# Optimization experiments

Measured on AMD Instinct MI355X. Metric: run time of the kernel, lower is better.

The kernel has to match this reference:

```python
import jax, jax.numpy as jnp
import numpy as np

EPS = 1e-5  # torch BatchNorm default

def _conv(x, w, pad):
    return jax.lax.conv_general_dilated(x, w, window_strides=(1, 1), padding=pad,
                                        dimension_numbers=('NCHW', 'OIHW', 'NCHW'))

def _bn(x, g, b, m, v):
    # eval-mode BatchNorm2d over channel axis 1 of NCHW
    scale = g / jnp.sqrt(v + EPS)
    return x * scale[None, :, None, None] + (b - m * scale)[None, :, None, None]

def _bn1d(x, g, b, m, v):
    scale = g / jnp.sqrt(v + EPS)
    return x * scale[None, :] + (b - m * scale)[None, :]

def _prelu(x, a):
    # torch PReLU with num_parameters=1 (scalar slope, init 0.25)
    return jnp.where(x >= 0, x, a * x)

def setup_inputs():
    key = jax.random.key(0)
    ks = jax.random.split(key, 10)
    B, H, W = 256, 600, 19
    C1, C2 = 40, 40
    x = jax.random.normal(ks[0], (B, H, W), jnp.float32)
    w1 = jax.random.normal(ks[1], (C1, 1, 29, 1), jnp.float32) * 0.1
    w2 = jax.random.normal(ks[2], (C2, C1, 1, 19), jnp.float32) * 0.1
    fc1_w = jax.random.uniform(ks[3], (80, 1560), jnp.float32, -0.005, 0.005)
    fc2_w = jax.random.uniform(ks[4], (2, 80), jnp.float32, -0.005, 0.005)
    def bn_params(k, n):
        k1, k2 = jax.random.split(k)
        return (jnp.ones((n,), jnp.float32), jnp.zeros((n,), jnp.float32),
                jax.random.normal(k1, (n,), jnp.float32) * 0.1,
                jax.random.uniform(k2, (n,), jnp.float32, 0.5, 1.5))
    bn1_g, bn1_b, bn1_m, bn1_v = bn_params(ks[5], C1)
    bn2_g, bn2_b, bn2_m, bn2_v = bn_params(ks[6], C2)
    bn3_g, bn3_b, bn3_m, bn3_v = bn_params(ks[7], 80)
    a1 = jnp.full((1,), 0.25, jnp.float32)
    a2 = jnp.full((1,), 0.25, jnp.float32)
    a3 = jnp.full((1,), 0.25, jnp.float32)
    return dict(x=x, w1=w1, bn1_g=bn1_g, bn1_b=bn1_b, bn1_m=bn1_m, bn1_v=bn1_v, a1=a1,
                w2=w2, bn2_g=bn2_g, bn2_b=bn2_b, bn2_m=bn2_m, bn2_v=bn2_v, a2=a2,
                fc1_w=fc1_w, bn3_g=bn3_g, bn3_b=bn3_b, bn3_m=bn3_m, bn3_v=bn3_v, a3=a3,
                fc2_w=fc2_w)

def reference(x, w1, bn1_g, bn1_b, bn1_m, bn1_v, a1,
              w2, bn2_g, bn2_b, bn2_m, bn2_v, a2,
              fc1_w, bn3_g, bn3_b, bn3_m, bn3_v, a3, fc2_w):
    h = x[:, None, :, :]                                  # [B,1,600,19]
    # conv1: inputs NOT binarized, weights sign-binarized
    h = _conv(h, jnp.sign(w1), [(14, 14), (0, 0)])         # [B,40,600,19]
    h = _prelu(_bn(h, bn1_g, bn1_b, bn1_m, bn1_v), a1)
    # conv2: inputs and weights binarized
    h = _conv(jnp.sign(h), jnp.sign(w2), [(0, 0), (0, 0)])  # [B,40,600,1]
    h = _prelu(_bn(h, bn2_g, bn2_b, bn2_m, bn2_v), a2)
    # AvgPool2d kernel (30,1) stride (15,1)
    h = jax.lax.reduce_window(h, 0.0, jax.lax.add, (1, 1, 30, 1), (1, 1, 15, 1), 'VALID') / 30.0  # [B,40,39,1]
    h = h.reshape(h.shape[0], -1)                          # [B,1560]
    # fc1: binarized input/weight; BatchNorm1d; PReLU; dropout is identity in eval
    h = jnp.sign(h) @ jnp.sign(fc1_w).T                    # [B,80]
    h = _prelu(_bn1d(h, bn3_g, bn3_b, bn3_m, bn3_v), a3)
    out = jnp.sign(h) @ jnp.sign(fc2_w).T                  # [B,2]
    return out
```

## Files before the change

kernel.cpp:

```cpp
#include <hip/hip_runtime.h>
#include <stdint.h>

#define B_ 256
#define H_ 600
#define W_ 19
#define C1_ 40
#define C2_ 40
#define KH_ 29
#define PAD_ 14
#define NW_ 760
#define NWORDS_ 12
#define NJ_ 39
#define FIN_ 1560
#define FOUT_ 80
#define FCW_ 25
#define XST2 328
#define HS_ 300

typedef float v2f __attribute__((ext_vector_type(2)));

__device__ __forceinline__ float fsgn(float x){ return (x > 0.f) ? 1.f : ((x < 0.f) ? -1.f : 0.f); }
__device__ __forceinline__ int8_t isgn(float x){ return (int8_t)((x > 0.f) - (x < 0.f)); }

__global__ void k0_setup(const float* __restrict__ w1, const float* __restrict__ w2,
                         const float* __restrict__ fc1w, const float* __restrict__ fc2w,
                         const float* __restrict__ g1, const float* __restrict__ b1,
                         const float* __restrict__ m1, const float* __restrict__ v1,
                         const float* __restrict__ g2, const float* __restrict__ b2,
                         const float* __restrict__ m2, const float* __restrict__ v2,
                         const float* __restrict__ g3, const float* __restrict__ b3,
                         const float* __restrict__ m3, const float* __restrict__ v3,
                         float* __restrict__ w1s, uint64_t* __restrict__ w2m,
                         uint64_t* __restrict__ fc1p, int8_t* __restrict__ fc2s,
                         float* __restrict__ bnp)
{
  int tid = blockIdx.x * blockDim.x + threadIdx.x;
  int np  = gridDim.x * blockDim.x;
  int lane = threadIdx.x & 63;
  int gw   = tid >> 6;
  int nw   = np >> 6;

  for (int i = tid; i < C1_*KH_; i += np) w1s[i] = fsgn(w1[i]);

  for (int v = gw; v < C2_*NWORDS_; v += nw){
    int c2 = v / NWORDS_, wd = v % NWORDS_;
    int idx = wd*64 + lane;
    float val = 0.f;
    if (idx < NW_){
      int c1 = idx % 40, w = idx / 40;
      val = w2[c2*NW_ + c1*W_ + w];
    }
    unsigned long long m = __ballot(val > 0.f);
    if (lane == 0) w2m[c2*NWORDS_ + wd] = m;
  }
  for (int v = gw; v < FOUT_*2*FCW_; v += nw){
    int o = v / (2*FCW_), r = v % (2*FCW_);
    int neg = r / FCW_, wd = r % FCW_;
    int e = wd*64 + lane;
    float val = (e < FIN_) ? fc1w[o*FIN_ + e] : 0.f;
    unsigned long long m = __ballot(neg ? (val < 0.f) : (val > 0.f));
    if (lane == 0) fc1p[o*(2*FCW_) + r] = m;
  }
  for (int i = tid; i < 2*FOUT_; i += np) fc2s[i] = isgn(fc2w[i]);
  for (int i = tid; i < C1_; i += np){
    float s = __fdiv_rn(g1[i], __fsqrt_rn(__fadd_rn(v1[i], 1e-5f)));
    bnp[i] = s; bnp[40+i] = __fsub_rn(b1[i], __fmul_rn(m1[i], s));
  }
  for (int i = tid; i < C2_; i += np){
    float s = __fdiv_rn(g2[i], __fsqrt_rn(__fadd_rn(v2[i], 1e-5f)));
    bnp[80+i] = s; bnp[120+i] = __fsub_rn(b2[i], __fmul_rn(m2[i], s));
  }
  for (int i = tid; i < FOUT_; i += np){
    float s = __fdiv_rn(g3[i], __fsqrt_rn(__fadd_rn(v3[i], 1e-5f)));
    bnp[160+i] = s; bnp[240+i] = __fsub_rn(b3[i], __fmul_rn(m3[i], s));
  }
}

#define FMA2(a,b,c) __builtin_elementwise_fma(a,b,c)
#define KE(k) { v2f wk = wt2[k]; \
  a0 = FMA2(wk, E[(k)/2+0], a0); a1 = FMA2(wk, E[(k)/2+1], a1); \
  a2 = FMA2(wk, E[(k)/2+2], a2); a3 = FMA2(wk, E[(k)/2+3], a3); \
  a4 = FMA2(wk, E[(k)/2+4], a4); a5 = FMA2(wk, E[(k)/2+5], a5); }
#define KO(k) { v2f wk = wt2[k]; \
  a0 = FMA2(wk, O[((k)-1)/2+0], a0); a1 = FMA2(wk, O[((k)-1)/2+1], a1); \
  a2 = FMA2(wk, O[((k)-1)/2+2], a2); a3 = FMA2(wk, O[((k)-1)/2+3], a3); \
  a4 = FMA2(wk, O[((k)-1)/2+4], a4); a5 = FMA2(wk, O[((k)-1)/2+5], a5); }

__global__ __launch_bounds__(768, 3) void k1_conv1(const float* __restrict__ x,
                                                   const float* __restrict__ w1s,
                                                   const float* __restrict__ bnp,
                                                   uint64_t* __restrict__ s1bits)
{
  __shared__ float xs[W_ * XST2];
  int b = blockIdx.x, t = blockIdx.y;
  int h0 = HS_ * t;
  const float* xb = x + (size_t)b * H_ * W_;
  for (int i = threadIdx.x; i < XST2 * W_; i += 768){
    int r = i / W_, w = i % W_;
    int gh = h0 - PAD_ + r;
    xs[w*XST2 + r] = (gh >= 0 && gh < H_) ? xb[gh*W_ + w] : 0.f;
  }
  __syncthreads();

  int tid  = threadIdx.x;
  int lane = tid & 63, wave = tid >> 6;
  bool valid = (tid < NW_);
  int c1 = tid % 40;
  int w  = valid ? (tid / 40) : 18;

  v2f wt2[KH_];
  #pragma unroll
  for (int k = 0; k < KH_; ++k){ float wv = w1s[c1*KH_ + k]; wt2[k] = (v2f){wv, wv}; }
  float scale = bnp[c1], bias = bnp[40 + c1];
  if (!valid){ scale = __builtin_nanf(""); bias = scale; }
  const float* xcol = &xs[w * XST2];
  uint64_t* bbase = s1bits + ((size_t)b * H_ + h0) * 24;

  for (int c = 0; c < 25; ++c){
    v2f E[20];
    const float4* xp = (const float4*)&xcol[12*c];
    #pragma unroll
    for (int q = 0; q < 10; ++q){
      float4 v = xp[q];
      E[2*q]   = (v2f){v.x, v.y};
      E[2*q+1] = (v2f){v.z, v.w};
    }
    v2f O[19];
    #pragma unroll
    for (int m = 0; m < 19; ++m) O[m] = (v2f){E[m].y, E[m+1].x};

    v2f a0 = (v2f)0.f, a1 = (v2f)0.f, a2 = (v2f)0.f,
        a3 = (v2f)0.f, a4 = (v2f)0.f, a5 = (v2f)0.f;
    KE(0)  KO(1)  KE(2)  KO(3)  KE(4)  KO(5)  KE(6)  KO(7)  KE(8)  KO(9)
    KE(10) KO(11) KE(12) KO(13) KE(14) KO(15) KE(16) KO(17) KE(18) KO(19)
    KE(20) KO(21) KE(22) KO(23) KE(24) KO(25) KE(26) KO(27) KE(28)

    v2f accs[6] = {a0, a1, a2, a3, a4, a5};
    #pragma unroll
    for (int j = 0; j < 6; ++j){
      float zx = __fadd_rn(__fmul_rn(accs[j].x, scale), bias);
      float zy = __fadd_rn(__fmul_rn(accs[j].y, scale), bias);
      unsigned long long px = __ballot(zx > 0.f);
      unsigned long long nx = __ballot(zx < 0.f);
      unsigned long long py = __ballot(zy > 0.f);
      unsigned long long ny = __ballot(zy < 0.f);
      if (lane == 0){
        int h = 12*c + 2*j;
        ulonglong2 v0; v0.x = px; v0.y = px | nx;
        ulonglong2 v1; v1.x = py; v1.y = py | ny;
        *(ulonglong2*)(bbase + (size_t)h     * 24 + wave*2) = v0;
        *(ulonglong2*)(bbase + (size_t)(h+1) * 24 + wave*2) = v1;
      }
    }
  }
}

__global__ __launch_bounds__(320) void k2_conv2pool(const uint64_t* __restrict__ s1bits,
                                                    const uint64_t* __restrict__ w2m_g,
                                                    const float* __restrict__ bnp,
                                                    const float* __restrict__ a2p,
                                                    int8_t* __restrict__ sp)
{
  __shared__ uint64_t st[135][NWORDS_][2];
  __shared__ int nz[136];
  int t = blockIdx.x, b = blockIdx.y;
  int j0 = 8*t;
  int nwin = NJ_ - j0; if (nwin > 8) nwin = 8;
  int r0 = 15*j0;
  int rows = H_ - r0; if (rows > 135) rows = 135;
  int tid = threadIdx.x;

  const ulonglong2* src = (const ulonglong2*)(s1bits + ((size_t)b * H_ + r0) * 24);
  ulonglong2* dst = (ulonglong2*)st;
  for (int i = tid; i < rows*NWORDS_; i += 320) dst[i] = src[i];
  __syncthreads();
  for (int r = tid; r < rows; r += 320){
    int s = 0;
    #pragma unroll
    for (int wd = 0; wd < NWORDS_; ++wd) s += __popcll(st[r][wd][1]);
    nz[r] = s;
  }
  __syncthreads();

  int c2 = tid % 40, jl = tid / 40;
  if (jl < nwin){
    uint64_t WP[NWORDS_];
    #pragma unroll
    for (int wd = 0; wd < NWORDS_; ++wd) WP[wd] = w2m_g[c2*NWORDS_ + wd];
    float s2 = bnp[c2], t2 = bnp[40 + c2], alpha = a2p[0];
    float psum = 0.f;
    int rbase = 15*jl;
    for (int rr = 0; rr < 30; ++rr){
      int r = rbase + rr;
      int d = 0;
      #pragma unroll
      for (int wd = 0; wd < NWORDS_; ++wd){
        ulonglong2 pm = *(const ulonglong2*)&st[r][wd][0];
        d += __popcll(pm.y & (pm.x ^ WP[wd]));
      }
      int y = nz[r] - 2*d;
      float u = __fadd_rn(__fmul_rn((float)y, s2), t2);
      float z = (u >= 0.f) ? u : __fmul_rn(alpha, u);
      psum = __fadd_rn(psum, z);
    }
    sp[(size_t)b * FIN_ + c2 * NJ_ + (j0 + jl)] = (int8_t)((psum > 0.f) - (psum < 0.f));
  }
}

__global__ __launch_bounds__(128) void k3_fc(const int8_t* __restrict__ sp,
                                             const uint64_t* __restrict__ fc1p,
                                             const int8_t* __restrict__ fc2s,
                                             const float* __restrict__ bnp,
                                             const float* __restrict__ a3p,
                                             float* __restrict__ out)
{
  __shared__ uint64_t spP[FCW_], spN[FCW_];
  __shared__ int z3[FOUT_];
  int b = blockIdx.x;
  int lane = threadIdx.x & 63, wave = threadIdx.x >> 6;
  const int8_t* spb = sp + (size_t)b * FIN_;
  for (int wd = wave; wd < FCW_; wd += 2){
    int e = wd*64 + lane;
    int v = (e < FIN_) ? (int)spb[e] : 0;
    unsigned long long p = __ballot(v > 0);
    unsigned long long n = __ballot(v < 0);
    if (lane == 0){ spP[wd] = p; spN[wd] = n; }
  }
  __syncthreads();
  float alpha = a3p[0];
  if (threadIdx.x < FOUT_){
    int o = threadIdx.x;
    const uint64_t* wp = fc1p + o * (2*FCW_);
    int acc = 0;
    #pragma unroll
    for (int wd = 0; wd < FCW_; ++wd){
      uint64_t P = spP[wd], N = spN[wd];
      uint64_t WP = wp[wd], WN = wp[FCW_ + wd];
      acc += __popcll(P & WP) + __popcll(N & WN) - __popcll(P & WN) - __popcll(N & WP);
    }
    float u = __fadd_rn(__fmul_rn((float)acc, bnp[o]), bnp[80 + o]);
    float z = (u >= 0.f) ? u : __fmul_rn(alpha, u);
    z3[o] = (z > 0.f) - (z < 0.f);
  }
  __syncthreads();
  if (threadIdx.x < 2){
    int k = threadIdx.x;
    int acc = 0;
    for (int o = 0; o < FOUT_; ++o) acc += z3[o] * (int)fc2s[k * FOUT_ + o];
    out[b*2 + k] = (float)acc;
  }
}

extern "C" void kernel_launch(void* const* d_in, const int* in_sizes, int n_in,
                              void* d_out, int out_size, void* d_ws, size_t ws_size,
                              hipStream_t stream)
{
  const float* x    = (const float*)d_in[0];
  const float* w1   = (const float*)d_in[1];
  const float* g1   = (const float*)d_in[2];
  const float* b1   = (const float*)d_in[3];
  const float* m1   = (const float*)d_in[4];
  const float* v1   = (const float*)d_in[5];
  const float* a1   = (const float*)d_in[6];   (void)a1;
  const float* w2   = (const float*)d_in[7];
  const float* g2   = (const float*)d_in[8];
  const float* b2   = (const float*)d_in[9];
  const float* m2   = (const float*)d_in[10];
  const float* v2   = (const float*)d_in[11];
  const float* a2   = (const float*)d_in[12];
  const float* fc1w = (const float*)d_in[13];
  const float* g3   = (const float*)d_in[14];
  const float* b3   = (const float*)d_in[15];
  const float* m3   = (const float*)d_in[16];
  const float* v3   = (const float*)d_in[17];
  const float* a3   = (const float*)d_in[18];
  const float* fc2w = (const float*)d_in[19];

  char* ws = (char*)d_ws;
  uint64_t* s1bits = (uint64_t*)(ws);
  uint64_t* w2m    = (uint64_t*)(ws + 29491200);
  float*    w1s    = (float*)   (ws + 29495040);
  float*    bnp    = (float*)   (ws + 29499680);
  int8_t*   sp     = (int8_t*)  (ws + 29500960);
  uint64_t* fc1p   = (uint64_t*)(ws + 29900320);
  int8_t*   fc2s   = (int8_t*)  (ws + 29932320);

  k0_setup<<<dim3(128), dim3(256), 0, stream>>>(w1, w2, fc1w, fc2w,
                                                g1, b1, m1, v1,
                                                g2, b2, m2, v2,
                                                g3, b3, m3, v3,
                                                w1s, w2m, fc1p, fc2s, bnp);
  k1_conv1<<<dim3(B_, 2), dim3(768), 0, stream>>>(x, w1s, bnp, s1bits);
  k2_conv2pool<<<dim3(5, B_), dim3(320), 0, stream>>>(s1bits, w2m, bnp + 80, a2, sp);
  k3_fc<<<dim3(B_), dim3(128), 0, stream>>>(sp, fc1p, fc2s, bnp + 160, a3, (float*)d_out);
}
```

Measured before the change: 244.5 us.

## Rework conv1 to rolling register window and conv2 to per-row threads

Conv1 drops the packed v2f six-output blocking and uses a scalar 29-tap rolling register window that loads one new input per output row, raising the occupancy hint to 6 waves. The shared-memory stride becomes odd to avoid bank conflicts. The s1bits layout changes to word-major per batch, and conv2 now gives one thread per row computing all 40 channels into shared memory, then pools in a separate pass. This removes the conv2 recomputation from overlapping pooling windows, at the cost of a large shared buffer, a block-wide sync, and scalar FMAs instead of packed ones in conv1.

```diff
diff --git a/kernel.cpp b/kernel.cpp
--- a/kernel.cpp
+++ b/kernel.cpp
@@ -14,10 +14,8 @@
 #define FIN_ 1560
 #define FOUT_ 80
 #define FCW_ 25
-#define XST2 328
+#define XST2 329
 #define HS_ 300
-
-typedef float v2f __attribute__((ext_vector_type(2)));
 
 __device__ __forceinline__ float fsgn(float x){ return (x > 0.f) ? 1.f : ((x < 0.f) ? -1.f : 0.f); }
 __device__ __forceinline__ int8_t isgn(float x){ return (int8_t)((x > 0.f) - (x < 0.f)); }
@@ -76,17 +74,30 @@
   }
 }
 
-#define FMA2(a,b,c) __builtin_elementwise_fma(a,b,c)
-#define KE(k) { v2f wk = wt2[k]; \
-  a0 = FMA2(wk, E[(k)/2+0], a0); a1 = FMA2(wk, E[(k)/2+1], a1); \
-  a2 = FMA2(wk, E[(k)/2+2], a2); a3 = FMA2(wk, E[(k)/2+3], a3); \
-  a4 = FMA2(wk, E[(k)/2+4], a4); a5 = FMA2(wk, E[(k)/2+5], a5); }
-#define KO(k) { v2f wk = wt2[k]; \
-  a0 = FMA2(wk, O[((k)-1)/2+0], a0); a1 = FMA2(wk, O[((k)-1)/2+1], a1); \
-  a2 = FMA2(wk, O[((k)-1)/2+2], a2); a3 = FMA2(wk, O[((k)-1)/2+3], a3); \
-  a4 = FMA2(wk, O[((k)-1)/2+4], a4); a5 = FMA2(wk, O[((k)-1)/2+5], a5); }
-
-__global__ __launch_bounds__(768, 3) void k1_conv1(const float* __restrict__ x,
+template<int T>
+__device__ __forceinline__ float acc29(float (&xw)[29], float (&wt)[29]){
+  float a = 0.f;
+  #pragma unroll
+  for (int k = 0; k < 29; ++k)
+    a = __builtin_fmaf(wt[k], xw[(T + k) % 29], a);
+  return a;
+}
+
+template<int T>
+__device__ __forceinline__ void step1(float (&xw)[29], float (&wt)[29],
+                                      const float* xck, ulonglong2* ob,
+                                      float scale, float bias, int lane){
+  xw[(T + 28) % 29] = xck[T + 28];
+  float acc = acc29<T>(xw, wt);
+  float z = __fadd_rn(__fmul_rn(acc, scale), bias);
+  unsigned long long pp = __ballot(z > 0.f);
+  unsigned long long nn = __ballot(z < 0.f);
+  if (lane == 0){ ulonglong2 v; v.x = pp; v.y = pp | nn; ob[T] = v; }
+}
+
+#define S1(t) step1<t>(xw, wt, xck, ob, scale, bias, lane);
+
+__global__ __launch_bounds__(768, 6) void k1_conv1(const float* __restrict__ x,
                                                    const float* __restrict__ w1s,
                                                    const float* __restrict__ bnp,
                                                    uint64_t* __restrict__ s1bits)
@@ -95,7 +106,7 @@
   int b = blockIdx.x, t = blockIdx.y;
   int h0 = HS_ * t;
   const float* xb = x + (size_t)b * H_ * W_;
-  for (int i = threadIdx.x; i < XST2 * W_; i += 768){
+  for (int i = threadIdx.x; i < (HS_ + 28) * W_; i += 768){
     int r = i / W_, w = i % W_;
     int gh = h0 - PAD_ + r;
     xs[w*XST2 + r] = (gh >= 0 && gh < H_) ? xb[gh*W_ + w] : 0.f;
@@ -108,102 +119,76 @@
   int c1 = tid % 40;
   int w  = valid ? (tid / 40) : 18;
 
-  v2f wt2[KH_];
-  #pragma unroll
-  for (int k = 0; k < KH_; ++k){ float wv = w1s[c1*KH_ + k]; wt2[k] = (v2f){wv, wv}; }
+  float wt[KH_];
+  #pragma unroll
+  for (int k = 0; k < KH_; ++k) wt[k] = w1s[c1*KH_ + k];
   float scale = bnp[c1], bias = bnp[40 + c1];
   if (!valid){ scale = __builtin_nanf(""); bias = scale; }
   const float* xcol = &xs[w * XST2];
-  uint64_t* bbase = s1bits + ((size_t)b * H_ + h0) * 24;
-
-  for (int c = 0; c < 25; ++c){
-    v2f E[20];
-    const float4* xp = (const float4*)&xcol[12*c];
-    #pragma unroll
-    for (int q = 0; q < 10; ++q){
-      float4 v = xp[q];
-      E[2*q]   = (v2f){v.x, v.y};
-      E[2*q+1] = (v2f){v.z, v.w};
-    }
-    v2f O[19];
-    #pragma unroll
-    for (int m = 0; m < 19; ++m) O[m] = (v2f){E[m].y, E[m+1].x};
-
-    v2f a0 = (v2f)0.f, a1 = (v2f)0.f, a2 = (v2f)0.f,
-        a3 = (v2f)0.f, a4 = (v2f)0.f, a5 = (v2f)0.f;
-    KE(0)  KO(1)  KE(2)  KO(3)  KE(4)  KO(5)  KE(6)  KO(7)  KE(8)  KO(9)
-    KE(10) KO(11) KE(12) KO(13) KE(14) KO(15) KE(16) KO(17) KE(18) KO(19)
-    KE(20) KO(21) KE(22) KO(23) KE(24) KO(25) KE(26) KO(27) KE(28)
-
-    v2f accs[6] = {a0, a1, a2, a3, a4, a5};
-    #pragma unroll
-    for (int j = 0; j < 6; ++j){
-      float zx = __fadd_rn(__fmul_rn(accs[j].x, scale), bias);
-      float zy = __fadd_rn(__fmul_rn(accs[j].y, scale), bias);
-      unsigned long long px = __ballot(zx > 0.f);
-      unsigned long long nx = __ballot(zx < 0.f);
-      unsigned long long py = __ballot(zy > 0.f);
-      unsigned long long ny = __ballot(zy < 0.f);
-      if (lane == 0){
-        int h = 12*c + 2*j;
-        ulonglong2 v0; v0.x = px; v0.y = px | nx;
-        ulonglong2 v1; v1.x = py; v1.y = py | ny;
-        *(ulonglong2*)(bbase + (size_t)h     * 24 + wave*2) = v0;
-        *(ulonglong2*)(bbase + (size_t)(h+1) * 24 + wave*2) = v1;
-      }
-    }
-  }
-}
-
-__global__ __launch_bounds__(320) void k2_conv2pool(const uint64_t* __restrict__ s1bits,
+
+  float xw[29];
+  #pragma unroll
+  for (int s = 0; s < 28; ++s) xw[s] = xcol[s];
+
+  ulonglong2* obase = (ulonglong2*)s1bits + ((size_t)(b*12 + wave) * H_ + h0);
+
+  #pragma unroll 1
+  for (int c = 0; c < 10; ++c){
+    const float* xck = xcol + 29*c;
+    ulonglong2* ob = obase + 29*c;
+    S1(0)  S1(1)  S1(2)  S1(3)  S1(4)  S1(5)  S1(6)  S1(7)  S1(8)  S1(9)
+    S1(10) S1(11) S1(12) S1(13) S1(14) S1(15) S1(16) S1(17) S1(18) S1(19)
+    S1(20) S1(21) S1(22) S1(23) S1(24) S1(25) S1(26) S1(27) S1(28)
+  }
+  {
+    const float* xck = xcol + 290;
+    ulonglong2* ob = obase + 290;
+    S1(0) S1(1) S1(2) S1(3) S1(4) S1(5) S1(6) S1(7) S1(8) S1(9)
+  }
+}
+
+__global__ __launch_bounds__(640) void k2_conv2pool(const uint64_t* __restrict__ s1bits,
                                                     const uint64_t* __restrict__ w2m_g,
                                                     const float* __restrict__ bnp,
                                                     const float* __restrict__ a2p,
                                                     int8_t* __restrict__ sp)
 {
-  __shared__ uint64_t st[135][NWORDS_][2];
-  __shared__ int nz[136];
-  int t = blockIdx.x, b = blockIdx.y;
-  int j0 = 8*t;
-  int nwin = NJ_ - j0; if (nwin > 8) nwin = 8;
-  int r0 = 15*j0;
-  int rows = H_ - r0; if (rows > 135) rows = 135;
+  __shared__ float z[C2_][640];
+  int b = blockIdx.x;
   int tid = threadIdx.x;
-
-  const ulonglong2* src = (const ulonglong2*)(s1bits + ((size_t)b * H_ + r0) * 24);
-  ulonglong2* dst = (ulonglong2*)st;
-  for (int i = tid; i < rows*NWORDS_; i += 320) dst[i] = src[i];
-  __syncthreads();
-  for (int r = tid; r < rows; r += 320){
-    int s = 0;
+  int rowc = (tid < H_) ? tid : (H_ - 1);
+
+  uint64_t Pv[NWORDS_], Mv[NWORDS_];
+  const ulonglong2* sb = (const ulonglong2*)s1bits + (size_t)b * NWORDS_ * H_;
+  #pragma unroll
+  for (int wd = 0; wd < NWORDS_; ++wd){
+    ulonglong2 pm = sb[(size_t)wd * H_ + rowc];
+    Pv[wd] = pm.x; Mv[wd] = pm.y;
+  }
+  int nzv = 0;
+  #pragma unroll
+  for (int wd = 0; wd < NWORDS_; ++wd) nzv += __popcll(Mv[wd]);
+
+  float alpha = a2p[0];
+  #pragma unroll 2
+  for (int c2 = 0; c2 < C2_; ++c2){
+    int dsum = 0;
     #pragma unroll
-    for (int wd = 0; wd < NWORDS_; ++wd) s += __popcll(st[r][wd][1]);
-    nz[r] = s;
-  }
-  __syncthreads();
-
-  int c2 = tid % 40, jl = tid / 40;
-  if (jl < nwin){
-    uint64_t WP[NWORDS_];
+    for (int wd = 0; wd < NWORDS_; ++wd)
+      dsum += __popcll(Mv[wd] & (Pv[wd] ^ w2m_g[c2*NWORDS_ + wd]));
+    int y = nzv - 2*dsum;
+    float u = __fadd_rn(__fmul_rn((float)y, bnp[c2]), bnp[40 + c2]);
+    z[c2][tid] = (u >= 0.f) ? u : __fmul_rn(alpha, u);
+  }
+  __syncthreads();
+
+  for (int o = tid; o < C2_*NJ_; o += 640){
+    int c2 = o / NJ_, j = o % NJ_;
+    float s = 0.f;
+    int base = 15*j;
     #pragma unroll
-    for (int wd = 0; wd < NWORDS_; ++wd) WP[wd] = w2m_g[c2*NWORDS_ + wd];
-    float s2 = bnp[c2], t2 = bnp[40 + c2], alpha = a2p[0];
-    float psum = 0.f;
-    int rbase = 15*jl;
-    for (int rr = 0; rr < 30; ++rr){
-      int r = rbase + rr;
-      int d = 0;
-      #pragma unroll
-      for (int wd = 0; wd < NWORDS_; ++wd){
-        ulonglong2 pm = *(const ulonglong2*)&st[r][wd][0];
-        d += __popcll(pm.y & (pm.x ^ WP[wd]));
-      }
-      int y = nz[r] - 2*d;
-      float u = __fadd_rn(__fmul_rn((float)y, s2), t2);
-      float z = (u >= 0.f) ? u : __fmul_rn(alpha, u);
-      psum = __fadd_rn(psum, z);
-    }
-    sp[(size_t)b * FIN_ + c2 * NJ_ + (j0 + jl)] = (int8_t)((psum > 0.f) - (psum < 0.f));
+    for (int r = 0; r < 30; ++r) s = __fadd_rn(s, z[c2][base + r]);
+    sp[(size_t)b*FIN_ + o] = (int8_t)((s > 0.f) - (s < 0.f));
   }
 }
 
@@ -291,6 +276,6 @@
                                                 g3, b3, m3, v3,
                                                 w1s, w2m, fc1p, fc2s, bnp);
   k1_conv1<<<dim3(B_, 2), dim3(768), 0, stream>>>(x, w1s, bnp, s1bits);
-  k2_conv2pool<<<dim3(5, B_), dim3(320), 0, stream>>>(s1bits, w2m, bnp + 80, a2, sp);
+  k2_conv2pool<<<dim3(B_), dim3(640), 0, stream>>>(s1bits, w2m, bnp + 80, a2, sp);
   k3_fc<<<dim3(B_), dim3(128), 0, stream>>>(sp, fc1p, fc2s, bnp + 160, a3, (float*)d_out);
 }
```

Result: faster. 219.9 us (-10.0%).
